# Performance work log

Hardware: AMD Instinct MI355X
Metric: run time of the kernel (lower is better)

## Reference

```python
import jax, jax.numpy as jnp
import numpy as np

N_S = 4096      # number of sentences
N_K = 8192      # number of knowledge entries
HID = 1024      # settings.hidden_dim
SENT = 1024     # settings.sent_dim


def setup_inputs() -> dict:
    key = jax.random.key(0)
    ks = jax.random.split(key, 6)
    sentences = jax.random.normal(ks[0], (N_S, SENT), dtype=jnp.float32)
    knowledge = jax.random.normal(ks[1], (N_K, 3 * HID), dtype=jnp.float32)
    # Linear params stored as [in, out] for x @ W + b
    Ws = jax.random.normal(ks[2], (SENT, HID), dtype=jnp.float32) * 0.02
    bs = jnp.zeros((HID,), dtype=jnp.float32)
    Wk = jax.random.normal(ks[3], (3 * HID, HID), dtype=jnp.float32) * 0.02
    bk = jnp.zeros((HID,), dtype=jnp.float32)
    return {"sentences": sentences, "knowledge": knowledge,
            "Ws": Ws, "bs": bs, "Wk": Wk, "bk": bk}


def reference(sentences, knowledge, Ws, bs, Wk, bk):
    S = sentences @ Ws + bs                  # [N_s, h]
    K = knowledge @ Wk + bk                  # [N_k, h]
    align_scores = S @ K.T                   # [N_s, N_k]
    # NOTE: softmax over dim=0 (sentence axis), exactly as the torch module
    attentions = jax.nn.softmax(align_scores, axis=0)
    fused = attentions @ knowledge           # [N_s, 3h]
    return (fused, attentions)
```

## Files before the change

### kernel.cpp

```cpp
#include <hip/hip_runtime.h>
#include <hip/hip_bf16.h>
#include <cstdint>
#include <cstddef>

#define N_S 4096
#define N_Kn 8192
#define HID 1024
#define SENT 1024
#define K3 3072

typedef __attribute__((ext_vector_type(4))) float f4;
typedef __attribute__((ext_vector_type(8))) short bf8;
typedef __attribute__((ext_vector_type(4))) short bf4;
typedef unsigned short u16;

__device__ __forceinline__ u16 f2bf(float x) {
    __hip_bfloat16 h = __float2bfloat16(x);
    return __builtin_bit_cast(u16, h);
}
__device__ __forceinline__ float bf2f(u16 u) {
    union { unsigned int u; float f; } v; v.u = ((unsigned int)u) << 16;
    return v.f;
}

__device__ __forceinline__ void gl16(const u16* g, u16* l) {
    __builtin_amdgcn_global_load_lds(
        (const __attribute__((address_space(1))) void*)g,
        (__attribute__((address_space(3))) void*)l, 16, 0, 0);
}

__device__ __forceinline__ int xcd_swz(int bid, int nwg) {
    const int cpx = nwg >> 3;
    return (bid & 7) * cpx + (bid >> 3);
}

__global__ __launch_bounds__(256) void transpose_split_f32(
    const float* __restrict__ in, u16* __restrict__ hi, u16* __restrict__ lo,
    int R, int C)
{
    __shared__ float tile[32][33];
    const int bx = blockIdx.x * 32, by = blockIdx.y * 32;
    const int tx = threadIdx.x & 31, ty = threadIdx.x >> 5;
#pragma unroll
    for (int i = 0; i < 32; i += 8)
        tile[ty + i][tx] = in[(size_t)(by + ty + i) * C + bx + tx];
    __syncthreads();
#pragma unroll
    for (int i = 0; i < 32; i += 8) {
        const float v = tile[tx][ty + i];
        const u16 h = f2bf(v);
        const size_t o = (size_t)(bx + ty + i) * R + by + tx;
        hi[o] = h;
        lo[o] = f2bf(v - bf2f(h));
    }
}

__global__ __launch_bounds__(256) void transpose_f32_bf16(
    const float* __restrict__ in, u16* __restrict__ out, int R, int C)
{
    __shared__ float tile[32][33];
    const int bx = blockIdx.x * 32, by = blockIdx.y * 32;
    const int tx = threadIdx.x & 31, ty = threadIdx.x >> 5;
#pragma unroll
    for (int i = 0; i < 32; i += 8)
        tile[ty + i][tx] = in[(size_t)(by + ty + i) * C + bx + tx];
    __syncthreads();
#pragma unroll
    for (int i = 0; i < 32; i += 8)
        out[(size_t)(bx + ty + i) * R + by + tx] = f2bf(tile[tx][ty + i]);
}

#define BARR __builtin_amdgcn_s_barrier()
#define PRIO1 __builtin_amdgcn_s_setprio(1)
#define PRIO0 __builtin_amdgcn_s_setprio(0)
#define VM7  asm volatile("s_waitcnt vmcnt(7)" ::: "memory")
#define VM0  asm volatile("s_waitcnt vmcnt(0)" ::: "memory")

#define GB_LDA(buf, mh) \
  _Pragma("unroll") for (int mf_ = 0; mf_ < 2; ++mf_) \
  _Pragma("unroll") for (int kk_ = 0; kk_ < 2; ++kk_) \
    fa[mf_][kk_] = *(const bf8*)&sA[buf][(wm*64 + ((mh)*2+mf_)*16 + fr)*64 + (((kk_*4+kg) ^ (fr&7))<<3)];

#define GB_LDB(buf, nh, FB) \
  _Pragma("unroll") for (int nf_ = 0; nf_ < 3; ++nf_) \
  _Pragma("unroll") for (int kk_ = 0; kk_ < 2; ++kk_) \
    FB[nf_][kk_] = *(const bf8*)&sB[buf][(wn*96 + ((nh)*3+nf_)*16 + fr)*64 + (((kk_*4+kg) ^ (fr&7))<<3)];

#define GB_MMA(mh, nh, FB) \
  _Pragma("unroll") for (int kk_ = 0; kk_ < 2; ++kk_) \
  _Pragma("unroll") for (int mf_ = 0; mf_ < 2; ++mf_) \
  _Pragma("unroll") for (int nf_ = 0; nf_ < 3; ++nf_) \
    acc[(mh)*2+mf_][(nh)*3+nf_] = __builtin_amdgcn_mfma_f32_16x16x32_bf16( \
        fa[mf_][kk_], FB[nf_][kk_], acc[(mh)*2+mf_][(nh)*3+nf_], 0, 0, 0);

__global__ __launch_bounds__(512, 2) void gemm8b(
    const u16* __restrict__ A, const u16* __restrict__ B,
    float* __restrict__ C, int N, int Kd, int gx)
{
    __shared__ u16 sA[2][256 * 64];
    __shared__ u16 sB[2][192 * 64];

    const int swz = xcd_swz(blockIdx.x, gridDim.x);
    const int bx = swz % gx, by = swz / gx;
    const long brow = (long)by * 256, bcol = (long)bx * 192;

    const int t = threadIdx.x;
    const int w = t >> 6, l = t & 63;
    const int fr = l & 15, kg = l >> 4;
    const int wm = w >> 1;
    const int wn = w & 1;

    const int srow = t >> 3;
    const int schk = ((t & 7) ^ (srow & 7)) << 3;
    const int sldb = w << 9;

    auto stA = [&](int buf, int s, int kt) {
        gl16(A + (brow + s * 64 + srow) * (long)Kd + ((long)kt << 6) + schk,
             &sA[buf][s * 4096 + sldb]);
    };
    auto stB = [&](int buf, int s, int kt) {
        gl16(B + (bcol + s * 64 + srow) * (long)Kd + ((long)kt << 6) + schk,
             &sB[buf][s * 4096 + sldb]);
    };

    f4 acc[4][6];
#pragma unroll
    for (int m = 0; m < 4; ++m)
#pragma unroll
        for (int n = 0; n < 6; ++n) acc[m][n] = (f4){0.f, 0.f, 0.f, 0.f};

    bf8 fa[2][2], fb0[3][2], fb1[3][2];

    const int NK = Kd >> 6;

    stB(0, 0, 0); stB(0, 1, 0); stB(0, 2, 0);
    stA(0, 0, 0); stA(0, 1, 0); stA(0, 2, 0); stA(0, 3, 0);
    stB(1, 0, 1); stB(1, 1, 1); stB(1, 2, 1);
    stA(1, 0, 1); stA(1, 1, 1); stA(1, 2, 1); stA(1, 3, 1);
    VM7;
    BARR;
    GB_LDB(0, 0, fb0);

    for (int kt = 0; kt < NK; ++kt) {
        const int buf = kt & 1;
        const int t2 = kt + 2;
        const bool s2 = t2 < NK;
        const bool more = kt + 1 < NK;

        GB_LDA(buf, 0);
        BARR; PRIO1; GB_MMA(0, 0, fb0); PRIO0;

        GB_LDB(buf, 1, fb1);
        BARR; PRIO1; GB_MMA(0, 1, fb1); PRIO0;

        GB_LDA(buf, 1);
        if (s2) { stB(buf, 0, t2); stB(buf, 1, t2); stB(buf, 2, t2); }
        BARR; PRIO1; GB_MMA(1, 0, fb0); PRIO0;

        if (s2) { stA(buf, 0, t2); stA(buf, 1, t2); stA(buf, 2, t2); stA(buf, 3, t2); }
        if (s2) { VM7; } else { VM0; }
        BARR;
        if (more) { GB_LDB(buf ^ 1, 0, fb0); }
        PRIO1; GB_MMA(1, 1, fb1); PRIO0;
    }

#pragma unroll
    for (int n = 0; n < 6; ++n) {
        const long c = bcol + wn * 96 + n * 16 + fr;
#pragma unroll
        for (int m = 0; m < 4; ++m) {
            const long r0 = brow + wm * 64 + m * 16 + kg * 4;
#pragma unroll
            for (int r = 0; r < 4; ++r)
                C[(r0 + r) * (long)N + c] = acc[m][n][r];
        }
    }
}

template <bool SPLIT, bool AF32, bool EPIS>
__global__ __launch_bounds__(256) void gemm_mfma(
    const void* __restrict__ Aany, const u16* __restrict__ Alo_,
    const u16* __restrict__ Bhi_, const u16* __restrict__ Blo_,
    float* __restrict__ Cf, u16* __restrict__ Chi, u16* __restrict__ Clo,
    const float* __restrict__ bias, int N, int Kd, int gx)
{
    constexpr int SA = AF32 ? 48 : 32;
    __shared__ u16 sAh[128 * SA];
    __shared__ u16 sAl[SPLIT ? 128 * SA : 8];
    __shared__ u16 sBh[128 * 32];
    __shared__ u16 sBl[SPLIT ? 128 * 32 : 8];

    const int swz = xcd_swz(blockIdx.x, gridDim.x);
    const int nst_x = gx >> 2;
    const int st = swz >> 4, off = swz & 15;
    const int bxi = (st % nst_x) * 4 + (off & 3);
    const int byi = (st / nst_x) * 4 + (off >> 2);

    const int t = threadIdx.x;
    const int w = t >> 6;
    const int l = t & 63;
    const long brow = (long)byi * 128;
    const long bcol = (long)bxi * 128;

    const int grow = l >> 2;
    const int gcol = ((l & 3) ^ ((l >> 3) & 3)) * 8;

    const int wr = (w >> 1) * 64;
    const int wc = (w & 1) * 64;
    const int fr = l & 15;
    const int kg = l >> 4;
    const int kq = (kg ^ ((fr >> 1) & 3)) * 8;

    f4 acc[4][4];
#pragma unroll
    for (int m = 0; m < 4; m++)
#pragma unroll
        for (int n = 0; n < 4; n++) acc[m][n] = (f4){0.f, 0.f, 0.f, 0.f};

    const int nkt = Kd >> 5;
    for (int kt = 0; kt < nkt; ++kt) {
        const int k0 = kt * 32;

#pragma unroll
        for (int i = 0; i < 2; ++i) {
            const long r = bcol + i * 64 + w * 16 + grow;
            const int lb = i * 2048 + w * 512;
            gl16(Bhi_ + r * Kd + k0 + gcol, sBh + lb);
            if constexpr (SPLIT) gl16(Blo_ + r * Kd + k0 + gcol, sBl + lb);
        }

        if constexpr (!AF32) {
            const u16* Ahi = (const u16*)Aany;
#pragma unroll
            for (int i = 0; i < 2; ++i) {
                const long r = brow + i * 64 + w * 16 + grow;
                const int lb = i * 2048 + w * 512;
                gl16(Ahi + r * Kd + k0 + gcol, sAh + lb);
                if constexpr (SPLIT) gl16(Alo_ + r * Kd + k0 + gcol, sAl + lb);
            }
        } else {
            const float* Af = (const float*)Aany;
            const int ar = w * 8 + (l >> 3);
            const int cF = (l & 7) * 4;
#pragma unroll
            for (int j = 0; j < 4; ++j) {
                const int r = j * 32 + ar;
                const f4 v = *(const f4*)(Af + (brow + r) * (long)Kd + k0 + cF);
                u16 h[4], lw[4];
#pragma unroll
                for (int q = 0; q < 4; ++q) {
                    h[q] = f2bf(v[q]);
                    if constexpr (SPLIT) lw[q] = f2bf(v[q] - bf2f(h[q]));
                }
                *(bf4*)&sAh[r * SA + cF] = *(bf4*)h;
                if constexpr (SPLIT) *(bf4*)&sAl[r * SA + cF] = *(bf4*)lw;
            }
        }
        __syncthreads();

        bf8 fah[4], fbh[4], fal[4], fbl[4];
#pragma unroll
        for (int m = 0; m < 4; ++m) {
            if constexpr (AF32) {
                fah[m] = *(bf8*)&sAh[(wr + m * 16 + fr) * SA + kg * 8];
                if constexpr (SPLIT) fal[m] = *(bf8*)&sAl[(wr + m * 16 + fr) * SA + kg * 8];
            } else {
                fah[m] = *(bf8*)&sAh[(wr + m * 16 + fr) * 32 + kq];
                if constexpr (SPLIT) fal[m] = *(bf8*)&sAl[(wr + m * 16 + fr) * 32 + kq];
            }
            fbh[m] = *(bf8*)&sBh[(wc + m * 16 + fr) * 32 + kq];
            if constexpr (SPLIT) fbl[m] = *(bf8*)&sBl[(wc + m * 16 + fr) * 32 + kq];
        }
#pragma unroll
        for (int m = 0; m < 4; ++m)
#pragma unroll
            for (int n = 0; n < 4; ++n) {
                acc[m][n] = __builtin_amdgcn_mfma_f32_16x16x32_bf16(fah[m], fbh[n], acc[m][n], 0, 0, 0);
                if constexpr (SPLIT) {
                    acc[m][n] = __builtin_amdgcn_mfma_f32_16x16x32_bf16(fah[m], fbl[n], acc[m][n], 0, 0, 0);
                    acc[m][n] = __builtin_amdgcn_mfma_f32_16x16x32_bf16(fal[m], fbh[n], acc[m][n], 0, 0, 0);
                }
            }
        __syncthreads();
    }

#pragma unroll
    for (int n = 0; n < 4; ++n) {
        const long c = bcol + wc + n * 16 + fr;
        float bv = 0.f;
        if constexpr (EPIS) bv = bias[c];
#pragma unroll
        for (int m = 0; m < 4; ++m) {
            const long r0 = brow + wr + m * 16 + kg * 4;
#pragma unroll
            for (int r = 0; r < 4; ++r) {
                const float v = acc[m][n][r] + bv;
                if constexpr (EPIS) {
                    const u16 h = f2bf(v);
                    Chi[(r0 + r) * (long)N + c] = h;
                    Clo[(r0 + r) * (long)N + c] = f2bf(v - bf2f(h));
                } else {
                    Cf[(r0 + r) * (long)N + c] = v;
                }
            }
        }
    }
}

#define RCHUNK 128

__global__ __launch_bounds__(256) void softmax_partial(
    const float* __restrict__ align, float* __restrict__ pm, float* __restrict__ ps)
{
    const int col = blockIdx.x * 256 + threadIdx.x;
    const int r0 = blockIdx.y * RCHUNK;
    float m = -3.4e38f;
    for (int r = 0; r < RCHUNK; r++)
        m = fmaxf(m, align[(size_t)(r0 + r) * N_Kn + col]);
    float s = 0.f;
    for (int r = 0; r < RCHUNK; r++)
        s += __expf(align[(size_t)(r0 + r) * N_Kn + col] - m);
    pm[(size_t)blockIdx.y * N_Kn + col] = m;
    ps[(size_t)blockIdx.y * N_Kn + col] = s;
}

__global__ __launch_bounds__(256) void softmax_combine(
    const float* __restrict__ pm, const float* __restrict__ ps,
    float* __restrict__ fm, float* __restrict__ fsinv)
{
    const int col = blockIdx.x * 256 + threadIdx.x;
    float m = -3.4e38f;
#pragma unroll
    for (int i = 0; i < 32; i++) m = fmaxf(m, pm[(size_t)i * N_Kn + col]);
    float s = 0.f;
#pragma unroll
    for (int i = 0; i < 32; i++)
        s += ps[(size_t)i * N_Kn + col] * __expf(pm[(size_t)i * N_Kn + col] - m);
    fm[col] = m;
    fsinv[col] = 1.f / s;
}

__global__ __launch_bounds__(256) void softmax_norm(
    float* __restrict__ align, u16* __restrict__ abf,
    const float* __restrict__ fm, const float* __restrict__ fsinv)
{
    const int col = blockIdx.x * 256 + threadIdx.x;
    const int r0 = blockIdx.y * RCHUNK;
    const float m = fm[col], si = fsinv[col];
    for (int r = 0; r < RCHUNK; r++) {
        const size_t idx = (size_t)(r0 + r) * N_Kn + col;
        const float v = __expf(align[idx] - m) * si;
        align[idx] = v;
        abf[idx] = f2bf(v);
    }
}

extern "C" void kernel_launch(void* const* d_in, const int* in_sizes, int n_in,
                              void* d_out, int out_size, void* d_ws, size_t ws_size,
                              hipStream_t stream)
{
    const float* sentences = (const float*)d_in[0];
    const float* knowledge = (const float*)d_in[1];
    const float* Ws = (const float*)d_in[2];
    const float* bs = (const float*)d_in[3];
    const float* Wk = (const float*)d_in[4];
    const float* bk = (const float*)d_in[5];

    float* out_fused = (float*)d_out;
    float* out_attn = (float*)d_out + (size_t)N_S * K3;

    char* w = (char*)d_ws;
    u16* attn_bf = (u16*)w;
    u16* WsT_hi = (u16*)w; w += (size_t)HID * SENT * 2;
    u16* WsT_lo = (u16*)w; w += (size_t)HID * SENT * 2;
    u16* WkT_hi = (u16*)w; w += (size_t)HID * K3 * 2;
    u16* WkT_lo = (u16*)w; w += (size_t)HID * K3 * 2;
    u16* S_hi   = (u16*)w; w += (size_t)N_S * HID * 2;
    u16* S_lo   = (u16*)w; w += (size_t)N_S * HID * 2;
    u16* K_hi   = (u16*)w; w += (size_t)N_Kn * HID * 2;
    u16* K_lo   = (u16*)w; w += (size_t)N_Kn * HID * 2;
    u16* kT     = (u16*)w; w += (size_t)K3 * N_Kn * 2;
    float* pm   = (float*)w; w += (size_t)32 * N_Kn * 4;
    float* ps   = (float*)w; w += (size_t)32 * N_Kn * 4;
    float* fm   = (float*)w; w += (size_t)N_Kn * 4;
    float* fsv  = (float*)w; w += (size_t)N_Kn * 4;

    transpose_split_f32<<<dim3(HID / 32, SENT / 32), 256, 0, stream>>>(Ws, WsT_hi, WsT_lo, SENT, HID);
    transpose_split_f32<<<dim3(HID / 32, K3 / 32), 256, 0, stream>>>(Wk, WkT_hi, WkT_lo, K3, HID);
    transpose_f32_bf16<<<dim3(K3 / 32, N_Kn / 32), 256, 0, stream>>>(knowledge, kT, N_Kn, K3);

    gemm_mfma<true, true, true><<<(HID / 128) * (N_S / 128), 256, 0, stream>>>(
        sentences, nullptr, WsT_hi, WsT_lo, nullptr, S_hi, S_lo, bs, HID, SENT, HID / 128);

    gemm_mfma<true, true, true><<<(HID / 128) * (N_Kn / 128), 256, 0, stream>>>(
        knowledge, nullptr, WkT_hi, WkT_lo, nullptr, K_hi, K_lo, bk, HID, K3, HID / 128);

    gemm_mfma<true, false, false><<<(N_Kn / 128) * (N_S / 128), 256, 0, stream>>>(
        S_hi, S_lo, K_hi, K_lo, out_attn, nullptr, nullptr, nullptr, N_Kn, HID, N_Kn / 128);

    softmax_partial<<<dim3(N_Kn / 256, N_S / RCHUNK), 256, 0, stream>>>(out_attn, pm, ps);
    softmax_combine<<<dim3(N_Kn / 256), 256, 0, stream>>>(pm, ps, fm, fsv);
    softmax_norm<<<dim3(N_Kn / 256, N_S / RCHUNK), 256, 0, stream>>>(out_attn, attn_bf, fm, fsv);

    gemm8b<<<(K3 / 192) * (N_S / 256), 512, 0, stream>>>(
        attn_bf, kT, out_fused, K3, N_Kn, K3 / 192);
}
```

Measured before the change: 751.5 us.

## Add 512-thread split-bf16 GEMM for alignment scores with pointer-increment staging

Replaces the generic 256-thread split-precision GEMM for S@K^T with a new 256x128-tile, 512-thread kernel. It double-buffers hi/lo bf16 operands through direct global-to-LDS loads with swizzled layouts and interleaves the three-product split MFMA work with barriers and priority hints. The existing gemm8b is also changed to advance precomputed pointers instead of recomputing addresses on each load. The aim is better reuse and latency hiding in the scores GEMM, at the cost of more LDS and register pressure.

```diff
diff --git a/kernel.cpp b/kernel.cpp
--- a/kernel.cpp
+++ b/kernel.cpp
@@ -33,6 +33,13 @@
     const int cpx = nwg >> 3;
     return (bid & 7) * cpx + (bid >> 3);
 }
+
+#define BARR __builtin_amdgcn_s_barrier()
+#define PRIO1 __builtin_amdgcn_s_setprio(1)
+#define PRIO0 __builtin_amdgcn_s_setprio(0)
+#define VM7  asm volatile("s_waitcnt vmcnt(7)" ::: "memory")
+#define VM6  asm volatile("s_waitcnt vmcnt(6)" ::: "memory")
+#define VM0  asm volatile("s_waitcnt vmcnt(0)" ::: "memory")
 
 __global__ __launch_bounds__(256) void transpose_split_f32(
     const float* __restrict__ in, u16* __restrict__ hi, u16* __restrict__ lo,
@@ -70,12 +77,6 @@
         out[(size_t)(bx + ty + i) * R + by + tx] = f2bf(tile[tx][ty + i]);
 }
 
-#define BARR __builtin_amdgcn_s_barrier()
-#define PRIO1 __builtin_amdgcn_s_setprio(1)
-#define PRIO0 __builtin_amdgcn_s_setprio(0)
-#define VM7  asm volatile("s_waitcnt vmcnt(7)" ::: "memory")
-#define VM0  asm volatile("s_waitcnt vmcnt(0)" ::: "memory")
-
 #define GB_LDA(buf, mh) \
   _Pragma("unroll") for (int mf_ = 0; mf_ < 2; ++mf_) \
   _Pragma("unroll") for (int kk_ = 0; kk_ < 2; ++kk_) \
@@ -114,14 +115,31 @@
     const int schk = ((t & 7) ^ (srow & 7)) << 3;
     const int sldb = w << 9;
 
-    auto stA = [&](int buf, int s, int kt) {
-        gl16(A + (brow + s * 64 + srow) * (long)Kd + ((long)kt << 6) + schk,
-             &sA[buf][s * 4096 + sldb]);
+    const u16* pA0 = A + (brow +   0 + srow) * (long)Kd + schk;
+    const u16* pA1 = A + (brow +  64 + srow) * (long)Kd + schk;
+    const u16* pA2 = A + (brow + 128 + srow) * (long)Kd + schk;
+    const u16* pA3 = A + (brow + 192 + srow) * (long)Kd + schk;
+    const u16* pB0 = B + (bcol +   0 + srow) * (long)Kd + schk;
+    const u16* pB1 = B + (bcol +  64 + srow) * (long)Kd + schk;
+    const u16* pB2 = B + (bcol + 128 + srow) * (long)Kd + schk;
+
+    auto stB3 = [&](int buf) {
+        u16* base = &sB[buf][0];
+        gl16(pB0, base + sldb);
+        gl16(pB1, base + 4096 + sldb);
+        gl16(pB2, base + 8192 + sldb);
     };
-    auto stB = [&](int buf, int s, int kt) {
-        gl16(B + (bcol + s * 64 + srow) * (long)Kd + ((long)kt << 6) + schk,
-             &sB[buf][s * 4096 + sldb]);
+    auto stA4 = [&](int buf) {
+        u16* base = &sA[buf][0];
+        gl16(pA0, base + sldb);
+        gl16(pA1, base + 4096 + sldb);
+        gl16(pA2, base + 8192 + sldb);
+        gl16(pA3, base + 12288 + sldb);
     };
+    auto advance = [&]() {
+        pA0 += 64; pA1 += 64; pA2 += 64; pA3 += 64;
+        pB0 += 64; pB1 += 64; pB2 += 64;
+    };
 
     f4 acc[4][6];
 #pragma unroll
@@ -133,18 +151,15 @@
 
     const int NK = Kd >> 6;
 
-    stB(0, 0, 0); stB(0, 1, 0); stB(0, 2, 0);
-    stA(0, 0, 0); stA(0, 1, 0); stA(0, 2, 0); stA(0, 3, 0);
-    stB(1, 0, 1); stB(1, 1, 1); stB(1, 2, 1);
-    stA(1, 0, 1); stA(1, 1, 1); stA(1, 2, 1); stA(1, 3, 1);
+    stB3(0); stA4(0); advance();
+    stB3(1); stA4(1); advance();
     VM7;
     BARR;
     GB_LDB(0, 0, fb0);
 
     for (int kt = 0; kt < NK; ++kt) {
         const int buf = kt & 1;
-        const int t2 = kt + 2;
-        const bool s2 = t2 < NK;
+        const bool s2 = kt + 2 < NK;
         const bool more = kt + 1 < NK;
 
         GB_LDA(buf, 0);
@@ -154,19 +169,121 @@
         BARR; PRIO1; GB_MMA(0, 1, fb1); PRIO0;
 
         GB_LDA(buf, 1);
-        if (s2) { stB(buf, 0, t2); stB(buf, 1, t2); stB(buf, 2, t2); }
+        if (s2) { stB3(buf); }
         BARR; PRIO1; GB_MMA(1, 0, fb0); PRIO0;
 
-        if (s2) { stA(buf, 0, t2); stA(buf, 1, t2); stA(buf, 2, t2); stA(buf, 3, t2); }
-        if (s2) { VM7; } else { VM0; }
+        if (s2) { stA4(buf); VM7; } else { VM0; }
         BARR;
         if (more) { GB_LDB(buf ^ 1, 0, fb0); }
         PRIO1; GB_MMA(1, 1, fb1); PRIO0;
+        advance();
     }
 
 #pragma unroll
     for (int n = 0; n < 6; ++n) {
         const long c = bcol + wn * 96 + n * 16 + fr;
+#pragma unroll
+        for (int m = 0; m < 4; ++m) {
+            const long r0 = brow + wm * 64 + m * 16 + kg * 4;
+#pragma unroll
+            for (int r = 0; r < 4; ++r)
+                C[(r0 + r) * (long)N + c] = acc[m][n][r];
+        }
+    }
+}
+
+#define GS_LD(buf) \
+  _Pragma("unroll") for (int m_ = 0; m_ < 4; ++m_) { \
+    fah[m_] = *(const bf8*)&sAh[buf][(wm*64 + m_*16 + fr)*32 + kq]; \
+    fal[m_] = *(const bf8*)&sAl[buf][(wm*64 + m_*16 + fr)*32 + kq]; } \
+  _Pragma("unroll") for (int j_ = 0; j_ < 4; ++j_) { \
+    fbh[j_] = *(const bf8*)&sBh[buf][(wn*64 + j_*16 + fr)*32 + kq]; \
+    fbl[j_] = *(const bf8*)&sBl[buf][(wn*64 + j_*16 + fr)*32 + kq]; }
+
+#define GS_MMA(nlo) \
+  _Pragma("unroll") for (int m_ = 0; m_ < 4; ++m_) \
+  _Pragma("unroll") for (int j_ = 0; j_ < 2; ++j_) { \
+    const int n_ = (nlo)*2 + j_; \
+    acc[m_][n_] = __builtin_amdgcn_mfma_f32_16x16x32_bf16(fah[m_], fbh[n_], acc[m_][n_], 0, 0, 0); \
+    acc[m_][n_] = __builtin_amdgcn_mfma_f32_16x16x32_bf16(fah[m_], fbl[n_], acc[m_][n_], 0, 0, 0); \
+    acc[m_][n_] = __builtin_amdgcn_mfma_f32_16x16x32_bf16(fal[m_], fbh[n_], acc[m_][n_], 0, 0, 0); }
+
+__global__ __launch_bounds__(512, 2) void gemm8s(
+    const u16* __restrict__ Ah, const u16* __restrict__ Al,
+    const u16* __restrict__ Bh, const u16* __restrict__ Bl,
+    float* __restrict__ C, int N, int Kd)
+{
+    __shared__ u16 sAh[2][8192], sAl[2][8192];
+    __shared__ u16 sBh[2][4096], sBl[2][4096];
+
+    const int bid = blockIdx.x;
+    const int q = bid >> 3;
+    const int by = (bid & 7) * 2 + (q & 1);
+    const int bx = q >> 1;
+    const long brow = (long)by * 256, bcol = (long)bx * 128;
+
+    const int t = threadIdx.x;
+    const int w = t >> 6, l = t & 63;
+    const int fr = l & 15, kg = l >> 4;
+    const int wm = w >> 1;
+    const int wn = w & 1;
+    const int kq = (kg ^ ((fr >> 1) & 3)) << 3;
+
+    const int srow = t >> 2;
+    const int schk = ((t & 3) ^ ((t >> 3) & 3)) << 3;
+    const int sldb = w << 9;
+
+    const u16* pAh0 = Ah + (brow + srow) * (long)Kd + schk;
+    const u16* pAh1 = Ah + (brow + 128 + srow) * (long)Kd + schk;
+    const u16* pAl0 = Al + (brow + srow) * (long)Kd + schk;
+    const u16* pAl1 = Al + (brow + 128 + srow) * (long)Kd + schk;
+    const u16* pBh0 = Bh + (bcol + srow) * (long)Kd + schk;
+    const u16* pBl0 = Bl + (bcol + srow) * (long)Kd + schk;
+
+    auto stage6 = [&](int buf) {
+        gl16(pBh0, &sBh[buf][sldb]);
+        gl16(pBl0, &sBl[buf][sldb]);
+        gl16(pAh0, &sAh[buf][sldb]);
+        gl16(pAh1, &sAh[buf][4096 + sldb]);
+        gl16(pAl0, &sAl[buf][sldb]);
+        gl16(pAl1, &sAl[buf][4096 + sldb]);
+    };
+    auto advance = [&]() {
+        pAh0 += 32; pAh1 += 32; pAl0 += 32; pAl1 += 32;
+        pBh0 += 32; pBl0 += 32;
+    };
+
+    f4 acc[4][4];
+#pragma unroll
+    for (int m = 0; m < 4; ++m)
+#pragma unroll
+        for (int n = 0; n < 4; ++n) acc[m][n] = (f4){0.f, 0.f, 0.f, 0.f};
+
+    bf8 fah[4], fal[4], fbh[4], fbl[4];
+
+    const int NK = Kd >> 5;
+
+    stage6(0); advance();
+    stage6(1); advance();
+    VM6;
+    BARR;
+
+    for (int kt = 0; kt < NK; ++kt) {
+        const int buf = kt & 1;
+        const bool s2 = kt + 2 < NK;
+
+        GS_LD(buf);
+        BARR; PRIO1; GS_MMA(0); PRIO0;
+
+        if (s2) { stage6(buf); VM6; } else { VM0; }
+        BARR;
+        PRIO1; GS_MMA(1); PRIO0;
+        advance();
+    }
+
+#pragma unroll
+    for (int n = 0; n < 4; ++n) {
+        const long c = bcol + wn * 64 + n * 16 + fr;
 #pragma unroll
         for (int m = 0; m < 4; ++m) {
             const long r0 = brow + wm * 64 + m * 16 + kg * 4;
@@ -395,8 +512,8 @@
     gemm_mfma<true, true, true><<<(HID / 128) * (N_Kn / 128), 256, 0, stream>>>(
         knowledge, nullptr, WkT_hi, WkT_lo, nullptr, K_hi, K_lo, bk, HID, K3, HID / 128);
 
-    gemm_mfma<true, false, false><<<(N_Kn / 128) * (N_S / 128), 256, 0, stream>>>(
-        S_hi, S_lo, K_hi, K_lo, out_attn, nullptr, nullptr, nullptr, N_Kn, HID, N_Kn / 128);
+    gemm8s<<<(N_Kn / 128) * (N_S / 256), 512, 0, stream>>>(
+        S_hi, S_lo, K_hi, K_lo, out_attn, N_Kn, HID);
 
     softmax_partial<<<dim3(N_Kn / 256, N_S / RCHUNK), 256, 0, stream>>>(out_attn, pm, ps);
     softmax_combine<<<dim3(N_Kn / 256), 256, 0, stream>>>(pm, ps, fm, fsv);
```

Result: no change. 753.2 us (median of 2 runs) (+0.2%).
